# Kernel tuning notes

Hardware: AMD Instinct MI355X
Metric: run time of the kernel (lower is better)

Reference implementation:

```python
import jax, jax.numpy as jnp
import numpy as np

EPS = 1e-8
SQRT_EPS_LOSS = 1e-6


def setup_inputs() -> dict:
    key = jax.random.key(0)
    ks = jax.random.split(key, 8)
    n_vars, n_clauses, n_edges, n_graphs = 500_000, 2_000_000, 6_000_000, 256
    dim, k = 128, 8
    x = jax.random.normal(ks[0], (n_vars, dim), jnp.float32)
    polarity = jnp.where(jax.random.bernoulli(ks[1], 0.5, (n_edges,)), 1.0, -1.0).astype(jnp.float32)
    variable_indices = jax.random.randint(ks[2], (n_edges,), 0, n_vars)
    clause_indices = jax.random.randint(ks[3], (n_edges,), 0, n_clauses)
    clause_batch = jnp.sort(jax.random.randint(ks[4], (n_clauses,), 0, n_graphs))
    W1 = jax.random.normal(ks[5], (dim, dim), jnp.float32) / np.sqrt(dim).astype(np.float32)
    b1 = jnp.zeros((dim,), jnp.float32)
    W2 = jax.random.normal(ks[6], (dim, k), jnp.float32) / np.sqrt(dim).astype(np.float32)
    b2 = jnp.zeros((k,), jnp.float32)
    return dict(x=x, polarity=polarity, variable_indices=variable_indices,
                clause_indices=clause_indices, clause_batch=clause_batch,
                W1=W1, b1=b1, W2=W2, b2=b2, n_graphs=n_graphs)


def reference(x, polarity, variable_indices, clause_indices, clause_batch, W1, b1, W2, b2, n_graphs):
    n_clauses = clause_batch.shape[0]
    k = W2.shape[1]

    # variables_output MLP: Linear -> ReLU -> Linear, [n_vars, k]
    logits = jax.nn.relu(x @ W1 + b1) @ W2 + b2

    # softplus_mixed_loss: gather literals along edges, scatter-sum into clauses
    lit = logits[variable_indices] * polarity[:, None]                      # [E, k]
    clause_sum = jax.ops.segment_sum(jax.nn.softplus(lit), clause_indices,
                                     num_segments=n_clauses)                # [C, k]
    clause_val = jnp.exp(-clause_sum)
    per_clause_loss = clause_val * (-jnp.log(1.0 - clause_val + EPS))       # [C, k]

    # per-graph soft loss
    per_graph_loss = jax.ops.segment_sum(per_clause_loss, clause_batch,
                                         num_segments=n_graphs)             # [G, k]
    per_graph_loss = jnp.sqrt(per_graph_loss + SQRT_EPS_LOSS) - np.float32(np.sqrt(SQRT_EPS_LOSS))

    costs = jnp.square(jnp.arange(1, k + 1, dtype=jnp.float32))             # [k]
    sorted_desc = -jnp.sort(-per_graph_loss, axis=-1)                       # descending sort per graph
    logit_loss = jnp.sum(sorted_desc * costs) / jnp.sum(costs)              # scalar

    # hard assignment check
    logits_hard = jnp.where(logits > 0, 1.0, -1.0)
    edge_hard = logits_hard[variable_indices] * polarity[:, None]           # [E, k]
    clauses_hard = jax.ops.segment_max(edge_hard, clause_indices,
                                       num_segments=n_clauses)              # amax per clause
    graphs_hard = jax.ops.segment_min(clauses_hard, clause_batch,
                                      num_segments=n_graphs)                # amin per graph
    solved = jnp.any(graphs_hard > 0.5, axis=1)                             # [G] bool

    return logit_loss, solved
```

## Files before the change

kernel.cpp:

```cpp
#include <hip/hip_runtime.h>
#include <hip/hip_bf16.h>

#define DIM 128
#define K 8
#define EPS 1e-8f
#define SQRT_EPS 1e-6f

#define CB 512
#define CSHIFT 9
#define NBMAX 4096
#define MAXSLOT 32
#define SARR_CAP 2560

#define TV1 8192
#define NT1MAX 1024
#define NKV 512
#define VSH 10
#define TB 4096
#define MAXTV 4
#define NKC 64
#define TC 4096
#define MAXTC 32

typedef __attribute__((ext_vector_type(8))) short bf16x8;
typedef __attribute__((ext_vector_type(4))) float f32x4;

__device__ inline short bfc(float f) {
    union { __hip_bfloat16 h; short s; } u;
    u.h = __float2bfloat16(f);
    return u.s;
}

#define LDW 136
#define NW 8

__global__ __launch_bounds__(512) void prep_kernel(
    const float* __restrict__ W1, const float* __restrict__ W2,
    unsigned short* __restrict__ w1tg, unsigned short* __restrict__ w2tg)
{
    const int t = threadIdx.x;
    for (int i = t; i < DIM * DIM; i += 512) {
        int r = i >> 7, c = i & 127;
        w1tg[c * DIM + r] = (unsigned short)bfc(W1[i]);
    }
    for (int i = t; i < 16 * DIM; i += 512) {
        int c = i >> 7, j = i & 127;
        w2tg[c * DIM + j] = (c < 8) ? (unsigned short)bfc(W2[j * 8 + c])
                                    : (unsigned short)0;
    }
}

__global__ __launch_bounds__(512) void mlp_kernel(
    const float* __restrict__ x, const unsigned short* __restrict__ w1tg,
    const float* __restrict__ b1, const unsigned short* __restrict__ w2tg,
    const float* __restrict__ b2, uint2* __restrict__ lfp8, int n_vars)
{
    __shared__ __align__(16) short w1t[DIM][LDW];
    __shared__ __align__(16) short w2t[16][LDW];
    __shared__ __align__(16) short hlds[NW][16][LDW];
    __shared__ __align__(16) float lout[NW][16][8];

    const int t = threadIdx.x;
    const int wave = t >> 6, lane = t & 63;
    const int lr = lane & 15, lg = lane >> 4;

    for (int i = t; i < DIM * DIM / 8; i += 512) {
        int row = i >> 4, col8 = (i & 15) * 8;
        *(bf16x8*)&w1t[row][col8] = *(const bf16x8*)&w1tg[row * DIM + col8];
    }
    for (int i = t; i < 16 * DIM / 8; i += 512) {
        int row = i >> 4, col8 = (i & 15) * 8;
        *(bf16x8*)&w2t[row][col8] = *(const bf16x8*)&w2tg[row * DIM + col8];
    }
    __syncthreads();

    const int rbase = blockIdx.x * 256 + wave * 32;

    bf16x8 a[2][4];
    #pragma unroll
    for (int rt = 0; rt < 2; ++rt) {
        int row = rbase + rt * 16 + lr;
        bool ok = row < n_vars;
        const float* xp = x + (size_t)row * DIM + lg * 8;
        #pragma unroll
        for (int kt = 0; kt < 4; ++kt) {
            bf16x8 av = {0,0,0,0,0,0,0,0};
            if (ok) {
                float4 f0 = *(const float4*)(xp + kt * 32);
                float4 f1 = *(const float4*)(xp + kt * 32 + 4);
                av[0]=bfc(f0.x); av[1]=bfc(f0.y); av[2]=bfc(f0.z); av[3]=bfc(f0.w);
                av[4]=bfc(f1.x); av[5]=bfc(f1.y); av[6]=bfc(f1.z); av[7]=bfc(f1.w);
            }
            a[rt][kt] = av;
        }
    }

    bf16x8 bb[4];
    #pragma unroll
    for (int kt = 0; kt < 4; ++kt)
        bb[kt] = *(const bf16x8*)&w2t[lr][kt * 32 + lg * 8];
    float b2v = (lr < 8) ? b2[lr] : 0.f;

    #pragma unroll
    for (int rt = 0; rt < 2; ++rt) {
        #pragma unroll
        for (int n = 0; n < 8; ++n) {
            f32x4 acc = {0.f, 0.f, 0.f, 0.f};
            #pragma unroll
            for (int kt = 0; kt < 4; ++kt) {
                bf16x8 bf = *(const bf16x8*)&w1t[n * 16 + lr][kt * 32 + lg * 8];
                acc = __builtin_amdgcn_mfma_f32_16x16x32_bf16(a[rt][kt], bf, acc, 0, 0, 0);
            }
            float bcol = b1[n * 16 + lr];
            #pragma unroll
            for (int r = 0; r < 4; ++r) {
                float h = fmaxf(acc[r] + bcol, 0.f);
                hlds[wave][lg * 4 + r][n * 16 + lr] = bfc(h);
            }
        }
        f32x4 acc2 = {0.f, 0.f, 0.f, 0.f};
        #pragma unroll
        for (int kt = 0; kt < 4; ++kt) {
            bf16x8 af = *(const bf16x8*)&hlds[wave][lr][kt * 32 + lg * 8];
            acc2 = __builtin_amdgcn_mfma_f32_16x16x32_bf16(af, bb[kt], acc2, 0, 0, 0);
        }
        if (lr < 8) {
            #pragma unroll
            for (int r = 0; r < 4; ++r)
                lout[wave][lg * 4 + r][lr] = acc2[r] + b2v;
        }
        if (lane < 16) {
            int row = rbase + rt * 16 + lane;
            if (row < n_vars) {
                const float* f = lout[wave][lane];
                unsigned lo = 0u, hi = 0u;
                lo = __builtin_amdgcn_cvt_pk_fp8_f32(f[0], f[1], lo, false);
                lo = __builtin_amdgcn_cvt_pk_fp8_f32(f[2], f[3], lo, true);
                hi = __builtin_amdgcn_cvt_pk_fp8_f32(f[4], f[5], hi, false);
                hi = __builtin_amdgcn_cvt_pk_fp8_f32(f[6], f[7], hi, true);
                lfp8[row] = make_uint2(lo, hi);
            }
        }
    }
}


__global__ __launch_bounds__(256) void histV_kernel(
    const int* __restrict__ vi, unsigned* __restrict__ histV, int n_edges)
{
    __shared__ unsigned hl[NKV];
    const int t = threadIdx.x, b = blockIdx.x;
    for (int i = t; i < NKV; i += 256) hl[i] = 0u;
    __syncthreads();
    const int e0 = b * TV1, e1 = min(e0 + TV1, n_edges);
    for (int e = e0 + t; e < e1; e += 256)
        atomicAdd(&hl[((unsigned)vi[e]) >> VSH], 1u);
    __syncthreads();
    for (int i = t; i < NKV; i += 256) histV[(size_t)i * NT1MAX + b] = hl[i];
}

__global__ __launch_bounds__(256) void scanrowV_kernel(
    unsigned* __restrict__ hist, unsigned* __restrict__ btotal)
{
    const int t = threadIdx.x;
    const size_t base = (size_t)blockIdx.x * NT1MAX + t * 4;
    uint4 v = *(const uint4*)(hist + base);
    unsigned pre0 = 0, pre1 = v.x, pre2 = v.x + v.y, pre3 = v.x + v.y + v.z;
    unsigned run = pre3 + v.w;
    __shared__ unsigned ts[256];
    ts[t] = run;
    __syncthreads();
    for (int off = 1; off < 256; off <<= 1) {
        unsigned xv = (t >= off) ? ts[t - off] : 0u;
        __syncthreads();
        ts[t] += xv;
        __syncthreads();
    }
    unsigned ex = ts[t] - run;
    uint4 o = {ex + pre0, ex + pre1, ex + pre2, ex + pre3};
    *(uint4*)(hist + base) = o;
    if (t == 255) btotal[blockIdx.x] = ts[255];
}

__global__ void baseV_kernel(const unsigned* __restrict__ tv,
                             unsigned* __restrict__ bv)
{
    if (threadIdx.x == 0) {
        unsigned r = 0;
        for (int k = 0; k < NKV; ++k) { bv[k] = r; r += tv[k]; }
        bv[NKV] = r;
    }
}

__global__ __launch_bounds__(256) void scatterV_kernel(
    const int* __restrict__ ci, const int* __restrict__ vi,
    const float* __restrict__ pol, const unsigned* __restrict__ histV,
    const unsigned* __restrict__ baseV, unsigned* __restrict__ A, int n_edges)
{
    __shared__ unsigned sa[TV1];
    __shared__ unsigned short bmap[TV1];
    __shared__ unsigned h[NKV], lst[NKV], h2[NKV], gst[NKV];
    __shared__ unsigned ts[256];
    const int t = threadIdx.x, b = blockIdx.x;
    for (int i = t; i < NKV; i += 256) h[i] = 0u;
    __syncthreads();
    const int e0 = b * TV1, e1 = min(e0 + TV1, n_edges), n = e1 - e0;
    for (int e = e0 + t; e < e1; e += 256)
        atomicAdd(&h[((unsigned)vi[e]) >> VSH], 1u);
    __syncthreads();
    unsigned a0 = h[2 * t], a1 = h[2 * t + 1];
    unsigned run = a0 + a1;
    ts[t] = run;
    __syncthreads();
    for (int off = 1; off < 256; off <<= 1) {
        unsigned xv = (t >= off) ? ts[t - off] : 0u;
        __syncthreads();
        ts[t] += xv;
        __syncthreads();
    }
    unsigned ex = ts[t] - run;
    lst[2 * t] = ex; lst[2 * t + 1] = ex + a0;
    h2[2 * t] = ex;  h2[2 * t + 1] = ex + a0;
    __syncthreads();
    for (int e = e0 + t; e < e1; e += 256) {
        unsigned c = (unsigned)ci[e];
        unsigned v = (unsigned)vi[e];
        unsigned neg = (pol[e] < 0.f) ? 1u : 0u;
        unsigned k = v >> VSH;
        unsigned p = atomicAdd(&h2[k], 1u);
        sa[p] = c | (neg << 21) | ((v & ((1u << VSH) - 1u)) << 22);
        bmap[p] = (unsigned short)k;
    }
    for (int i = t; i < NKV; i += 256)
        gst[i] = baseV[i] + histV[(size_t)i * NT1MAX + b];
    __syncthreads();
    for (int s = t; s < n; s += 256) {
        unsigned k = bmap[s];
        A[gst[k] + (s - lst[k])] = sa[s];
    }
}


__global__ __launch_bounds__(256) void histB_kernel(
    const unsigned* __restrict__ A, const unsigned* __restrict__ baseV,
    unsigned* __restrict__ histB)
{
    __shared__ unsigned h[NKC];
    const int t = threadIdx.x;
    const int vg = blockIdx.x / MAXTV, i = blockIdx.x % MAXTV;
    const unsigned slo = baseV[vg], shi = baseV[vg + 1];
    const unsigned t0 = slo + (unsigned)i * TB;
    if (t0 >= shi) return;
    const unsigned t1 = min(t0 + TB, shi);
    if (t < NKC) h[t] = 0u;
    __syncthreads();
    for (unsigned e = t0 + t; e < t1; e += 256)
        atomicAdd(&h[(A[e] & 0x1FFFFFu) >> 15], 1u);
    __syncthreads();
    if (t < NKC) histB[(size_t)t * (NKV * MAXTV) + blockIdx.x] = h[t];
}

__global__ __launch_bounds__(256) void scanrowB_kernel(
    unsigned* __restrict__ hist, unsigned* __restrict__ btotal)
{
    const int t = threadIdx.x;
    const size_t base = (size_t)blockIdx.x * (NKV * MAXTV) + t * 8;
    uint4 v0 = *(const uint4*)(hist + base);
    uint4 v1 = *(const uint4*)(hist + base + 4);
    unsigned p0 = 0, p1 = v0.x, p2 = p1 + v0.y, p3 = p2 + v0.z, p4 = p3 + v0.w;
    unsigned p5 = p4 + v1.x, p6 = p5 + v1.y, p7 = p6 + v1.z;
    unsigned run = p7 + v1.w;
    __shared__ unsigned ts[256];
    ts[t] = run;
    __syncthreads();
    for (int off = 1; off < 256; off <<= 1) {
        unsigned xv = (t >= off) ? ts[t - off] : 0u;
        __syncthreads();
        ts[t] += xv;
        __syncthreads();
    }
    unsigned ex = ts[t] - run;
    uint4 o0 = {ex + p0, ex + p1, ex + p2, ex + p3};
    uint4 o1 = {ex + p4, ex + p5, ex + p6, ex + p7};
    *(uint4*)(hist + base) = o0;
    *(uint4*)(hist + base + 4) = o1;
    if (t == 255) btotal[blockIdx.x] = ts[255];
}

__global__ void baseB_kernel(const unsigned* __restrict__ tb,
                             unsigned* __restrict__ bb)
{
    if (threadIdx.x == 0) {
        unsigned r = 0;
        for (int k = 0; k < NKC; ++k) { bb[k] = r; r += tb[k]; }
        bb[NKC] = r;
    }
}

__global__ __launch_bounds__(256) void scatterB_kernel(
    const unsigned* __restrict__ A, const uint2* __restrict__ lfp8,
    const unsigned* __restrict__ baseV, const unsigned* __restrict__ histB,
    const unsigned* __restrict__ baseB, unsigned short* __restrict__ B1,
    uint2* __restrict__ B2, int n_vars)
{
    __shared__ uint2 slice[1 << VSH];
    __shared__ unsigned short st1[TB];
    __shared__ uint2 st2[TB];
    __shared__ unsigned char bmap[TB];
    __shared__ unsigned h[NKC], lst[NKC], h2[NKC], gst[NKC];
    const int t = threadIdx.x;
    const int vg = blockIdx.x / MAXTV, i = blockIdx.x % MAXTV;
    const unsigned slo = baseV[vg], shi = baseV[vg + 1];
    const unsigned t0 = slo + (unsigned)i * TB;
    if (t0 >= shi) return;
    const unsigned t1 = min(t0 + TB, shi);
    const int n = (int)(t1 - t0);
    for (int s = t; s < (1 << VSH); s += 256) {
        int v = (vg << VSH) + s;
        slice[s] = (v < n_vars) ? lfp8[v] : make_uint2(0u, 0u);
    }
    if (t < NKC) h[t] = 0u;
    __syncthreads();
    for (unsigned e = t0 + t; e < t1; e += 256)
        atomicAdd(&h[(A[e] & 0x1FFFFFu) >> 15], 1u);
    __syncthreads();
    if (t == 0) {
        unsigned r = 0;
        for (int k = 0; k < NKC; ++k) { lst[k] = r; h2[k] = r; r += h[k]; }
    }
    __syncthreads();
    for (unsigned e = t0 + t; e < t1; e += 256) {
        unsigned a = A[e];
        unsigned c = a & 0x1FFFFFu;
        unsigned k = c >> 15;
        unsigned p = atomicAdd(&h2[k], 1u);
        uint2 g = slice[a >> 22];
        unsigned sm = ((a >> 21) & 1u) * 0x80808080u;
        g.x ^= sm; g.y ^= sm;
        st1[p] = (unsigned short)(c & 0x7FFFu);
        st2[p] = g;
        bmap[p] = (unsigned char)k;
    }
    if (t < NKC) gst[t] = baseB[t] + histB[(size_t)t * (NKV * MAXTV) + blockIdx.x];
    __syncthreads();
    for (int s = t; s < n; s += 256) {
        unsigned k = bmap[s];
        unsigned pos = gst[k] + (s - lst[k]);
        B1[pos] = st1[s];
        B2[pos] = st2[s];
    }
}


__global__ __launch_bounds__(256) void histC_kernel(
    const unsigned short* __restrict__ B1, const unsigned* __restrict__ baseB,
    unsigned* __restrict__ histC)
{
    __shared__ unsigned h[64];
    const int t = threadIdx.x;
    const int k1 = blockIdx.x / MAXTC, i = blockIdx.x % MAXTC;
    const unsigned slo = baseB[k1], shi = baseB[k1 + 1];
    const unsigned t0 = slo + (unsigned)i * TC;
    if (t0 >= shi) return;
    const unsigned t1 = min(t0 + TC, shi);
    if (t < 64) h[t] = 0u;
    __syncthreads();
    for (unsigned e = t0 + t; e < t1; e += 256)
        atomicAdd(&h[((unsigned)B1[e] >> 9) & 63u], 1u);
    __syncthreads();
    if (t < 64) histC[(size_t)(k1 * 64 + t) * MAXTC + i] = h[t];
}

__global__ __launch_bounds__(256) void scanrowC_kernel(
    unsigned* __restrict__ histC, unsigned* __restrict__ ctotal)
{
    const int rid = blockIdx.x * 256 + threadIdx.x;
    unsigned r = 0;
    for (int i = 0; i < MAXTC; ++i) {
        unsigned v = histC[(size_t)rid * MAXTC + i];
        histC[(size_t)rid * MAXTC + i] = r;
        r += v;
    }
    ctotal[rid] = r;
}

__global__ __launch_bounds__(256) void bbase_kernel(
    const unsigned* __restrict__ ctotal, unsigned* __restrict__ bbase, int nb)
{
    const int t = threadIdx.x;
    unsigned loc[16];
    unsigned run = 0;
    #pragma unroll
    for (int it = 0; it < 16; ++it) {
        int idx = t * 16 + it;
        unsigned v = (idx < 4096) ? ctotal[idx] : 0u;
        loc[it] = run;
        run += v;
    }
    __shared__ unsigned ts[256];
    ts[t] = run;
    __syncthreads();
    for (int off = 1; off < 256; off <<= 1) {
        unsigned xv = (t >= off) ? ts[t - off] : 0u;
        __syncthreads();
        ts[t] += xv;
        __syncthreads();
    }
    unsigned ex = ts[t] - run;
    #pragma unroll
    for (int it = 0; it < 16; ++it) {
        int idx = t * 16 + it;
        if (idx <= nb) bbase[idx] = ex + loc[it];
    }
}

__global__ __launch_bounds__(256) void scatterC_kernel(
    const unsigned short* __restrict__ B1, const uint2* __restrict__ B2,
    const unsigned* __restrict__ baseB, const unsigned* __restrict__ histC,
    const unsigned* __restrict__ bbase, unsigned short* __restrict__ sortedS,
    uint2* __restrict__ sortedL)
{
    __shared__ unsigned short st1[TC];
    __shared__ uint2 st2[TC];
    __shared__ unsigned char bmap[TC];
    __shared__ unsigned h[64], lst[64], h2[64], gst[64];
    const int t = threadIdx.x;
    const int k1 = blockIdx.x / MAXTC, i = blockIdx.x % MAXTC;
    const unsigned slo = baseB[k1], shi = baseB[k1 + 1];
    const unsigned t0 = slo + (unsigned)i * TC;
    if (t0 >= shi) return;
    const unsigned t1 = min(t0 + TC, shi);
    const int n = (int)(t1 - t0);
    if (t < 64) h[t] = 0u;
    __syncthreads();
    for (unsigned e = t0 + t; e < t1; e += 256)
        atomicAdd(&h[((unsigned)B1[e] >> 9) & 63u], 1u);
    __syncthreads();
    if (t == 0) {
        unsigned r = 0;
        for (int k = 0; k < 64; ++k) { lst[k] = r; h2[k] = r; r += h[k]; }
    }
    __syncthreads();
    for (unsigned e = t0 + t; e < t1; e += 256) {
        unsigned b = (unsigned)B1[e];
        unsigned k2 = (b >> 9) & 63u;
        unsigned p = atomicAdd(&h2[k2], 1u);
        st1[p] = (unsigned short)(b & 0x1FFu);
        st2[p] = B2[e];
        bmap[p] = (unsigned char)k2;
    }
    if (t < 64) {
        unsigned cbk = (unsigned)(k1 * 64 + t);
        gst[t] = bbase[cbk] + histC[(size_t)cbk * MAXTC + i];
    }
    __syncthreads();
    for (int s = t; s < n; s += 256) {
        unsigned k = bmap[s];
        unsigned pos = gst[k] + (s - lst[k]);
        sortedS[pos] = st1[s];
        sortedL[pos] = st2[s];
    }
}

__global__ __launch_bounds__(256) void bucket_kernel(
    const unsigned short* __restrict__ sortedS, const uint2* __restrict__ sortedL,
    const unsigned* __restrict__ bbase, const int* __restrict__ clause_batch,
    float* __restrict__ per_graph, unsigned* __restrict__ gmask,
    int n_clauses, int n_graphs)
{
    __shared__ uint2 sarrL[SARR_CAP];
    __shared__ unsigned cnt[CB];
    __shared__ unsigned cst[CB + 1];
    __shared__ float sp[256];
    __shared__ float pg[MAXSLOT * K];
    __shared__ unsigned pmask[MAXSLOT];
    __shared__ unsigned wtot[4];
    __shared__ int sh_ghi;

    const int t = threadIdx.x;
    const int lane = t & 63, wv = t >> 6;
    const int bkt = blockIdx.x;
    const int c_base = bkt << CSHIFT;
    const int n_cl = min(CB, n_clauses - c_base);
    const int g_lo = clause_batch[c_base];

    {
        float v = __builtin_amdgcn_cvt_f32_fp8((unsigned)t, 0);
        sp[t] = fmaxf(v, 0.f) + __logf(1.f + __expf(-fabsf(v)));
    }
    for (int i = t; i < CB; i += 256) cnt[i] = 0u;
    for (int i = t; i < MAXSLOT * K; i += 256) pg[i] = 0.f;
    if (t < MAXSLOT) pmask[t] = 0xFFu;
    if (t == 0) sh_ghi = clause_batch[c_base + n_cl - 1];
    __syncthreads();

    const unsigned lo = bbase[bkt], hi = bbase[bkt + 1];
    const int ne = (int)(hi - lo);

    float loss0[K], loss1[K];
    unsigned msk0 = 0u, msk1 = 0u;
    bool have0 = false, have1 = false;

    if (ne <= SARR_CAP) {
        for (unsigned e = lo + t; e < hi; e += 256)
            atomicAdd(&cnt[sortedS[e] & 511u], 1u);
        __syncthreads();
        unsigned a0 = cnt[2 * t], a1 = cnt[2 * t + 1];
        unsigned run = a0 + a1;
        unsigned incl = run;
        #pragma unroll
        for (int off = 1; off < 64; off <<= 1) {
            unsigned v = __shfl_up(incl, off, 64);
            if (lane >= off) incl += v;
        }
        if (lane == 63) wtot[wv] = incl;
        __syncthreads();
        unsigned wpre = 0;
        #pragma unroll
        for (int w = 0; w < 3; ++w) if (w < wv) wpre += wtot[w];
        unsigned ex = wpre + incl - run;
        cst[2 * t] = ex; cst[2 * t + 1] = ex + a0;
        cnt[2 * t] = ex; cnt[2 * t + 1] = ex + a0;
        if (t == 255) cst[CB] = ex + run;
        __syncthreads();
        for (unsigned e = lo + t; e < hi; e += 256) {
            unsigned cl = sortedS[e] & 511u;
            unsigned p = atomicAdd(&cnt[cl], 1u);
            sarrL[p] = sortedL[e];
        }
        __syncthreads();
        #pragma unroll
        for (int oc = 0; oc < 2; ++oc) {
            int cl = 2 * t + oc;
            if (cl >= n_cl) continue;
            unsigned s0 = cst[cl];
            int n = (int)(cst[cl + 1] - s0);
            float sums[K] = {0.f, 0.f, 0.f, 0.f, 0.f, 0.f, 0.f, 0.f};
            unsigned ormask = 0u;
            for (int base = 0; base < n; base += 8) {
                int m = min(8, n - base);
                uint2 gs[8];
                for (int i2 = 0; i2 < m; ++i2) gs[i2] = sarrL[s0 + base + i2];
                for (int i2 = 0; i2 < m; ++i2) {
                    #pragma unroll
                    for (int j = 0; j < 4; ++j) {
                        unsigned b0 = (gs[i2].x >> (8 * j)) & 0xFFu;
                        unsigned b1 = (gs[i2].y >> (8 * j)) & 0xFFu;
                        sums[j]     += sp[b0];
                        sums[j + 4] += sp[b1];
                        ormask |= (b0 - 1u < 0x7Fu) ? (1u << j) : 0u;
                        ormask |= (b1 - 1u < 0x7Fu) ? (1u << (j + 4)) : 0u;
                    }
                }
            }
            float* lss = oc ? loss1 : loss0;
            #pragma unroll
            for (int j = 0; j < K; ++j) {
                float cv = __expf(-sums[j]);
                lss[j] = cv * (-__logf(1.f - cv + EPS));
            }
            if (oc) { msk1 = ormask; have1 = true; }
            else    { msk0 = ormask; have0 = true; }
        }
    } else {
        float* acc = (float*)sarrL;
        unsigned* fmsk = cnt;
        for (int i = t; i < CB * K; i += 256) acc[i] = 0.f;
        for (int i = t; i < CB; i += 256) fmsk[i] = 0u;
        __syncthreads();
        for (unsigned e = lo + t; e < hi; e += 256) {
            unsigned cl = sortedS[e] & 511u;
            uint2 g = sortedL[e];
            unsigned gt0 = 0u;
            #pragma unroll
            for (int j = 0; j < 4; ++j) {
                unsigned b0 = (g.x >> (8 * j)) & 0xFFu;
                unsigned b1 = (g.y >> (8 * j)) & 0xFFu;
                atomicAdd(&acc[cl * K + j], sp[b0]);
                atomicAdd(&acc[cl * K + j + 4], sp[b1]);
                gt0 |= (b0 - 1u < 0x7Fu) ? (1u << j) : 0u;
                gt0 |= (b1 - 1u < 0x7Fu) ? (1u << (j + 4)) : 0u;
            }
            atomicOr(&fmsk[cl], gt0);
        }
        __syncthreads();
        #pragma unroll
        for (int oc = 0; oc < 2; ++oc) {
            int cl = 2 * t + oc;
            if (cl >= n_cl) continue;
            float* lss = oc ? loss1 : loss0;
            #pragma unroll
            for (int j = 0; j < K; ++j) {
                float cv = __expf(-acc[cl * K + j]);
                lss[j] = cv * (-__logf(1.f - cv + EPS));
            }
            if (oc) { msk1 = fmsk[cl]; have1 = true; }
            else    { msk0 = fmsk[cl]; have0 = true; }
        }
    }

    if (have0) {
        int slot0 = clause_batch[c_base + 2 * t] - g_lo;
        int slot1 = have1 ? (clause_batch[c_base + 2 * t + 1] - g_lo) : -1;
        if (have1 && slot1 == slot0) {
            #pragma unroll
            for (int j = 0; j < K; ++j) loss0[j] += loss1[j];
            msk0 &= msk1;
            have1 = false;
        }
        if (slot0 < MAXSLOT) {
            #pragma unroll
            for (int j = 0; j < K; ++j) atomicAdd(&pg[slot0 * K + j], loss0[j]);
            atomicAnd(&pmask[slot0], msk0);
        } else {
            #pragma unroll
            for (int j = 0; j < K; ++j) atomicAdd(&per_graph[(size_t)(g_lo + slot0) * K + j], loss0[j]);
            atomicAnd(&gmask[g_lo + slot0], msk0);
        }
        if (have1) {
            if (slot1 < MAXSLOT) {
                #pragma unroll
                for (int j = 0; j < K; ++j) atomicAdd(&pg[slot1 * K + j], loss1[j]);
                atomicAnd(&pmask[slot1], msk1);
            } else {
                #pragma unroll
                for (int j = 0; j < K; ++j) atomicAdd(&per_graph[(size_t)(g_lo + slot1) * K + j], loss1[j]);
                atomicAnd(&gmask[g_lo + slot1], msk1);
            }
        }
    }
    __syncthreads();

    const int nslots = min(sh_ghi - g_lo + 1, MAXSLOT);
    if (t < nslots * K) {
        int s = t >> 3, j = t & 7;
        atomicAdd(&per_graph[(size_t)(g_lo + s) * K + j], pg[s * K + j]);
    }
    if (t < nslots) atomicAnd(&gmask[g_lo + t], pmask[t]);
}

__global__ __launch_bounds__(256) void final_kernel(
    const float* __restrict__ per_graph, const unsigned* __restrict__ gmask,
    int n_graphs, float* __restrict__ out)
{
    const int t = threadIdx.x;
    float dot = 0.f;
    if (t < n_graphs) {
        float v[K];
        #pragma unroll
        for (int j = 0; j < K; ++j)
            v[j] = sqrtf(per_graph[(size_t)t * K + j] + SQRT_EPS) - sqrtf(SQRT_EPS);
        #pragma unroll
        for (int i = 1; i < K; ++i) {
            float key = v[i];
            int j = i - 1;
            while (j >= 0 && v[j] < key) { v[j + 1] = v[j]; --j; }
            v[j + 1] = key;
        }
        #pragma unroll
        for (int i = 0; i < K; ++i)
            dot = fmaf(v[i], (float)((i + 1) * (i + 1)), dot);
        out[1 + t] = (gmask[t] & 0xFFu) ? 1.f : 0.f;
    }
    __shared__ float red[256];
    red[t] = dot;
    __syncthreads();
    for (int s = 128; s >= 1; s >>= 1) {
        if (t < s) red[t] += red[t + s];
        __syncthreads();
    }
    if (t == 0) out[0] = red[0] * (1.f / 204.f);
}

extern "C" void kernel_launch(void* const* d_in, const int* in_sizes, int n_in,
                              void* d_out, int out_size, void* d_ws, size_t ws_size,
                              hipStream_t stream) {
    const float* x   = (const float*)d_in[0];
    const float* pol = (const float*)d_in[1];
    const int* vi    = (const int*)d_in[2];
    const int* ci    = (const int*)d_in[3];
    const int* cb    = (const int*)d_in[4];
    const float* W1  = (const float*)d_in[5];
    const float* b1  = (const float*)d_in[6];
    const float* W2  = (const float*)d_in[7];
    const float* b2  = (const float*)d_in[8];

    const int n_vars    = in_sizes[0] / DIM;
    const int n_edges   = in_sizes[1];
    const int n_clauses = in_sizes[4];
    const int n_graphs  = out_size - 1;
    const int nb        = (n_clauses + CB - 1) / CB;
    const int nt1       = (n_edges + TV1 - 1) / TV1;

    char* ws = (char*)d_ws;
    size_t off = 0;
    auto alloc = [&](size_t bytes) { char* p = ws + off; off += (bytes + 255) & ~(size_t)255; return p; };
    uint2*    lfp8   = (uint2*)alloc((size_t)n_vars * 8);
    unsigned* A      = (unsigned*)alloc((size_t)n_edges * 4);
    unsigned short* B1 = (unsigned short*)alloc((size_t)n_edges * 2);
    uint2*    B2     = (uint2*)alloc((size_t)n_edges * 8);
    uint2*    sortedL= (uint2*)alloc((size_t)n_edges * 8);
    unsigned* histV  = (unsigned*)alloc((size_t)NKV * NT1MAX * 4);
    unsigned* histB  = (unsigned*)alloc((size_t)NKC * NKV * MAXTV * 4);
    unsigned* histC  = (unsigned*)alloc((size_t)4096 * MAXTC * 4);
    unsigned* btotalV= (unsigned*)alloc((size_t)(NKV + 1) * 4);
    unsigned* baseV  = (unsigned*)alloc((size_t)(NKV + 1) * 4);
    unsigned* btotalB= (unsigned*)alloc((size_t)(NKC + 1) * 4);
    unsigned* baseB  = (unsigned*)alloc((size_t)(NKC + 1) * 4);
    unsigned* ctotal = (unsigned*)alloc((size_t)4096 * 4);
    unsigned* bbase  = (unsigned*)alloc((size_t)(NBMAX + 1) * 4);
    float*    per_graph = (float*)alloc((size_t)n_graphs * K * 4);
    unsigned* gmask  = (unsigned*)alloc((size_t)n_graphs * 4);
    unsigned short* w1tg = (unsigned short*)alloc((size_t)DIM * DIM * 2);
    unsigned short* w2tg = (unsigned short*)alloc((size_t)16 * DIM * 2);
    unsigned short* sortedS = (unsigned short*)A;

    hipMemsetAsync(histV, 0, (size_t)NKV * NT1MAX * 4, stream);
    hipMemsetAsync(histB, 0, (size_t)NKC * NKV * MAXTV * 4, stream);
    hipMemsetAsync(histC, 0, (size_t)4096 * MAXTC * 4, stream);
    hipMemsetAsync(per_graph, 0, (size_t)n_graphs * K * 4, stream);
    hipMemsetAsync(gmask, 0xFF, (size_t)n_graphs * 4, stream);

    prep_kernel<<<1, 512, 0, stream>>>(W1, W2, w1tg, w2tg);
    mlp_kernel<<<(n_vars + 255) / 256, 512, 0, stream>>>(x, w1tg, b1, w2tg, b2,
                                                         lfp8, n_vars);

    histV_kernel<<<nt1, 256, 0, stream>>>(vi, histV, n_edges);
    scanrowV_kernel<<<NKV, 256, 0, stream>>>(histV, btotalV);
    baseV_kernel<<<1, 64, 0, stream>>>(btotalV, baseV);
    scatterV_kernel<<<nt1, 256, 0, stream>>>(ci, vi, pol, histV, baseV, A, n_edges);

    histB_kernel<<<NKV * MAXTV, 256, 0, stream>>>(A, baseV, histB);
    scanrowB_kernel<<<NKC, 256, 0, stream>>>(histB, btotalB);
    baseB_kernel<<<1, 64, 0, stream>>>(btotalB, baseB);
    scatterB_kernel<<<NKV * MAXTV, 256, 0, stream>>>(A, lfp8, baseV, histB, baseB,
                                                     B1, B2, n_vars);

    histC_kernel<<<NKC * MAXTC, 256, 0, stream>>>(B1, baseB, histC);
    scanrowC_kernel<<<16, 256, 0, stream>>>(histC, ctotal);
    bbase_kernel<<<1, 256, 0, stream>>>(ctotal, bbase, nb);
    scatterC_kernel<<<NKC * MAXTC, 256, 0, stream>>>(B1, B2, baseB, histC, bbase,
                                                     sortedS, sortedL);

    bucket_kernel<<<nb, 256, 0, stream>>>(sortedS, sortedL, bbase, cb,
                                          per_graph, gmask, n_clauses, n_graphs);
    final_kernel<<<1, 256, 0, stream>>>(per_graph, gmask, n_graphs, (float*)d_out);
}
```

Before: 456.5 us.

## Halve clause bucket and sort tile sizes to increase block-level parallelism

Shrinks the clause bucket from 512 to 256 clauses, so each thread in the bucket kernel handles one clause instead of two. It also halves the edge tiles in the three radix-sort passes, doubling block counts and widening the per-pass histograms and scans to match. The MLP kernel now reads W2 straight from global memory instead of staging it in shared memory. The aim is more blocks and less shared memory per block for better occupancy, at the cost of more partial histograms to scan and more per-graph atomics from smaller buckets.

```diff
diff --git a/kernel.cpp b/kernel.cpp
--- a/kernel.cpp
+++ b/kernel.cpp
@@ -6,21 +6,22 @@
 #define EPS 1e-8f
 #define SQRT_EPS 1e-6f
 
-#define CB 512
-#define CSHIFT 9
-#define NBMAX 4096
+#define CB 256
+#define CSHIFT 8
+#define NBMAX 8192
 #define MAXSLOT 32
-#define SARR_CAP 2560
-
-#define TV1 8192
-#define NT1MAX 1024
+#define SARR_CAP 1280
+
+#define TV1 4096
+#define NT1MAX 2048
 #define NKV 512
 #define VSH 10
-#define TB 4096
-#define MAXTV 4
+#define TB 2048
+#define MAXTV 8
 #define NKC 64
-#define TC 4096
-#define MAXTC 32
+#define TC 2048
+#define MAXTC 64
+#define NFB 128
 
 typedef __attribute__((ext_vector_type(8))) short bf16x8;
 typedef __attribute__((ext_vector_type(4))) float f32x4;
@@ -56,7 +57,6 @@
     const float* __restrict__ b2, uint2* __restrict__ lfp8, int n_vars)
 {
     __shared__ __align__(16) short w1t[DIM][LDW];
-    __shared__ __align__(16) short w2t[16][LDW];
     __shared__ __align__(16) short hlds[NW][16][LDW];
     __shared__ __align__(16) float lout[NW][16][8];
 
@@ -67,10 +67,6 @@
     for (int i = t; i < DIM * DIM / 8; i += 512) {
         int row = i >> 4, col8 = (i & 15) * 8;
         *(bf16x8*)&w1t[row][col8] = *(const bf16x8*)&w1tg[row * DIM + col8];
-    }
-    for (int i = t; i < 16 * DIM / 8; i += 512) {
-        int row = i >> 4, col8 = (i & 15) * 8;
-        *(bf16x8*)&w2t[row][col8] = *(const bf16x8*)&w2tg[row * DIM + col8];
     }
     __syncthreads();
 
@@ -98,7 +94,7 @@
     bf16x8 bb[4];
     #pragma unroll
     for (int kt = 0; kt < 4; ++kt)
-        bb[kt] = *(const bf16x8*)&w2t[lr][kt * 32 + lg * 8];
+        bb[kt] = *(const bf16x8*)&w2tg[lr * DIM + kt * 32 + lg * 8];
     float b2v = (lr < 8) ? b2[lr] : 0.f;
 
     #pragma unroll
@@ -163,10 +159,12 @@
     unsigned* __restrict__ hist, unsigned* __restrict__ btotal)
 {
     const int t = threadIdx.x;
-    const size_t base = (size_t)blockIdx.x * NT1MAX + t * 4;
-    uint4 v = *(const uint4*)(hist + base);
-    unsigned pre0 = 0, pre1 = v.x, pre2 = v.x + v.y, pre3 = v.x + v.y + v.z;
-    unsigned run = pre3 + v.w;
+    const size_t base = (size_t)blockIdx.x * NT1MAX + t * 8;
+    uint4 v0 = *(const uint4*)(hist + base);
+    uint4 v1 = *(const uint4*)(hist + base + 4);
+    unsigned p0 = 0, p1 = v0.x, p2 = p1 + v0.y, p3 = p2 + v0.z, p4 = p3 + v0.w;
+    unsigned p5 = p4 + v1.x, p6 = p5 + v1.y, p7 = p6 + v1.z;
+    unsigned run = p7 + v1.w;
     __shared__ unsigned ts[256];
     ts[t] = run;
     __syncthreads();
@@ -177,8 +175,10 @@
         __syncthreads();
     }
     unsigned ex = ts[t] - run;
-    uint4 o = {ex + pre0, ex + pre1, ex + pre2, ex + pre3};
-    *(uint4*)(hist + base) = o;
+    uint4 o0 = {ex + p0, ex + p1, ex + p2, ex + p3};
+    uint4 o1 = {ex + p4, ex + p5, ex + p6, ex + p7};
+    *(uint4*)(hist + base) = o0;
+    *(uint4*)(hist + base + 4) = o1;
     if (t == 255) btotal[blockIdx.x] = ts[255];
 }
 
@@ -264,12 +264,17 @@
     unsigned* __restrict__ hist, unsigned* __restrict__ btotal)
 {
     const int t = threadIdx.x;
-    const size_t base = (size_t)blockIdx.x * (NKV * MAXTV) + t * 8;
-    uint4 v0 = *(const uint4*)(hist + base);
-    uint4 v1 = *(const uint4*)(hist + base + 4);
-    unsigned p0 = 0, p1 = v0.x, p2 = p1 + v0.y, p3 = p2 + v0.z, p4 = p3 + v0.w;
-    unsigned p5 = p4 + v1.x, p6 = p5 + v1.y, p7 = p6 + v1.z;
-    unsigned run = p7 + v1.w;
+    const size_t base = (size_t)blockIdx.x * (NKV * MAXTV) + t * 16;
+    unsigned v[16];
+    #pragma unroll
+    for (int q = 0; q < 4; ++q) {
+        uint4 vv = *(const uint4*)(hist + base + q * 4);
+        v[q*4+0]=vv.x; v[q*4+1]=vv.y; v[q*4+2]=vv.z; v[q*4+3]=vv.w;
+    }
+    unsigned pre[16];
+    unsigned run = 0;
+    #pragma unroll
+    for (int q = 0; q < 16; ++q) { pre[q] = run; run += v[q]; }
     __shared__ unsigned ts[256];
     ts[t] = run;
     __syncthreads();
@@ -280,10 +285,11 @@
         __syncthreads();
     }
     unsigned ex = ts[t] - run;
-    uint4 o0 = {ex + p0, ex + p1, ex + p2, ex + p3};
-    uint4 o1 = {ex + p4, ex + p5, ex + p6, ex + p7};
-    *(uint4*)(hist + base) = o0;
-    *(uint4*)(hist + base + 4) = o1;
+    #pragma unroll
+    for (int q = 0; q < 4; ++q) {
+        uint4 o = {ex + pre[q*4+0], ex + pre[q*4+1], ex + pre[q*4+2], ex + pre[q*4+3]};
+        *(uint4*)(hist + base + q * 4) = o;
+    }
     if (t == 255) btotal[blockIdx.x] = ts[255];
 }
 
@@ -356,19 +362,19 @@
     const unsigned short* __restrict__ B1, const unsigned* __restrict__ baseB,
     unsigned* __restrict__ histC)
 {
-    __shared__ unsigned h[64];
+    __shared__ unsigned h[NFB];
     const int t = threadIdx.x;
     const int k1 = blockIdx.x / MAXTC, i = blockIdx.x % MAXTC;
     const unsigned slo = baseB[k1], shi = baseB[k1 + 1];
     const unsigned t0 = slo + (unsigned)i * TC;
     if (t0 >= shi) return;
     const unsigned t1 = min(t0 + TC, shi);
-    if (t < 64) h[t] = 0u;
+    if (t < NFB) h[t] = 0u;
     __syncthreads();
     for (unsigned e = t0 + t; e < t1; e += 256)
-        atomicAdd(&h[((unsigned)B1[e] >> 9) & 63u], 1u);
-    __syncthreads();
-    if (t < 64) histC[(size_t)(k1 * 64 + t) * MAXTC + i] = h[t];
+        atomicAdd(&h[((unsigned)B1[e] >> CSHIFT) & (NFB - 1u)], 1u);
+    __syncthreads();
+    if (t < NFB) histC[(size_t)(k1 * NFB + t) * MAXTC + i] = h[t];
 }
 
 __global__ __launch_bounds__(256) void scanrowC_kernel(
@@ -388,12 +394,12 @@
     const unsigned* __restrict__ ctotal, unsigned* __restrict__ bbase, int nb)
 {
     const int t = threadIdx.x;
-    unsigned loc[16];
+    unsigned loc[32];
     unsigned run = 0;
     #pragma unroll
-    for (int it = 0; it < 16; ++it) {
-        int idx = t * 16 + it;
-        unsigned v = (idx < 4096) ? ctotal[idx] : 0u;
+    for (int it = 0; it < 32; ++it) {
+        int idx = t * 32 + it;
+        unsigned v = (idx < 8192) ? ctotal[idx] : 0u;
         loc[it] = run;
         run += v;
     }
@@ -408,8 +414,8 @@
     }
     unsigned ex = ts[t] - run;
     #pragma unroll
-    for (int it = 0; it < 16; ++it) {
-        int idx = t * 16 + it;
+    for (int it = 0; it < 32; ++it) {
+        int idx = t * 32 + it;
         if (idx <= nb) bbase[idx] = ex + loc[it];
     }
 }
@@ -423,7 +429,7 @@
     __shared__ unsigned short st1[TC];
     __shared__ uint2 st2[TC];
     __shared__ unsigned char bmap[TC];
-    __shared__ unsigned h[64], lst[64], h2[64], gst[64];
+    __shared__ unsigned h[NFB], lst[NFB], h2[NFB], gst[NFB];
     const int t = threadIdx.x;
     const int k1 = blockIdx.x / MAXTC, i = blockIdx.x % MAXTC;
     const unsigned slo = baseB[k1], shi = baseB[k1 + 1];
@@ -431,26 +437,26 @@
     if (t0 >= shi) return;
     const unsigned t1 = min(t0 + TC, shi);
     const int n = (int)(t1 - t0);
-    if (t < 64) h[t] = 0u;
+    if (t < NFB) h[t] = 0u;
     __syncthreads();
     for (unsigned e = t0 + t; e < t1; e += 256)
-        atomicAdd(&h[((unsigned)B1[e] >> 9) & 63u], 1u);
+        atomicAdd(&h[((unsigned)B1[e] >> CSHIFT) & (NFB - 1u)], 1u);
     __syncthreads();
     if (t == 0) {
         unsigned r = 0;
-        for (int k = 0; k < 64; ++k) { lst[k] = r; h2[k] = r; r += h[k]; }
+        for (int k = 0; k < NFB; ++k) { lst[k] = r; h2[k] = r; r += h[k]; }
     }
     __syncthreads();
     for (unsigned e = t0 + t; e < t1; e += 256) {
         unsigned b = (unsigned)B1[e];
-        unsigned k2 = (b >> 9) & 63u;
+        unsigned k2 = (b >> CSHIFT) & (NFB - 1u);
         unsigned p = atomicAdd(&h2[k2], 1u);
-        st1[p] = (unsigned short)(b & 0x1FFu);
+        st1[p] = (unsigned short)(b & (CB - 1u));
         st2[p] = B2[e];
         bmap[p] = (unsigned char)k2;
     }
-    if (t < 64) {
-        unsigned cbk = (unsigned)(k1 * 64 + t);
+    if (t < NFB) {
+        unsigned cbk = (unsigned)(k1 * NFB + t);
         gst[t] = bbase[cbk] + histC[(size_t)cbk * MAXTC + i];
     }
     __syncthreads();
@@ -488,26 +494,25 @@
         float v = __builtin_amdgcn_cvt_f32_fp8((unsigned)t, 0);
         sp[t] = fmaxf(v, 0.f) + __logf(1.f + __expf(-fabsf(v)));
     }
-    for (int i = t; i < CB; i += 256) cnt[i] = 0u;
+    cnt[t] = 0u;
+    if (t < MAXSLOT) { pmask[t] = 0xFFu; }
     for (int i = t; i < MAXSLOT * K; i += 256) pg[i] = 0.f;
-    if (t < MAXSLOT) pmask[t] = 0xFFu;
     if (t == 0) sh_ghi = clause_batch[c_base + n_cl - 1];
     __syncthreads();
 
     const unsigned lo = bbase[bkt], hi = bbase[bkt + 1];
     const int ne = (int)(hi - lo);
 
-    float loss0[K], loss1[K];
-    unsigned msk0 = 0u, msk1 = 0u;
-    bool have0 = false, have1 = false;
+    float loss0[K];
+    unsigned msk0 = 0u;
+    bool have0 = false;
 
     if (ne <= SARR_CAP) {
         for (unsigned e = lo + t; e < hi; e += 256)
-            atomicAdd(&cnt[sortedS[e] & 511u], 1u);
-        __syncthreads();
-        unsigned a0 = cnt[2 * t], a1 = cnt[2 * t + 1];
-        unsigned run = a0 + a1;
-        unsigned incl = run;
+            atomicAdd(&cnt[sortedS[e] & (CB - 1u)], 1u);
+        __syncthreads();
+        unsigned a0 = cnt[t];
+        unsigned incl = a0;
         #pragma unroll
         for (int off = 1; off < 64; off <<= 1) {
             unsigned v = __shfl_up(incl, off, 64);
@@ -518,23 +523,20 @@
         unsigned wpre = 0;
         #pragma unroll
         for (int w = 0; w < 3; ++w) if (w < wv) wpre += wtot[w];
-        unsigned ex = wpre + incl - run;
-        cst[2 * t] = ex; cst[2 * t + 1] = ex + a0;
-        cnt[2 * t] = ex; cnt[2 * t + 1] = ex + a0;
-        if (t == 255) cst[CB] = ex + run;
+        unsigned ex = wpre + incl - a0;
+        cst[t] = ex;
+        cnt[t] = ex;
+        if (t == 255) cst[CB] = ex + a0;
         __syncthreads();
         for (unsigned e = lo + t; e < hi; e += 256) {
-            unsigned cl = sortedS[e] & 511u;
+            unsigned cl = sortedS[e] & (CB - 1u);
             unsigned p = atomicAdd(&cnt[cl], 1u);
             sarrL[p] = sortedL[e];
         }
         __syncthreads();
-        #pragma unroll
-        for (int oc = 0; oc < 2; ++oc) {
-            int cl = 2 * t + oc;
-            if (cl >= n_cl) continue;
-            unsigned s0 = cst[cl];
-            int n = (int)(cst[cl + 1] - s0);
+        if (t < n_cl) {
+            unsigned s0 = cst[t];
+            int n = (int)(cst[t + 1] - s0);
             float sums[K] = {0.f, 0.f, 0.f, 0.f, 0.f, 0.f, 0.f, 0.f};
             unsigned ormask = 0u;
             for (int base = 0; base < n; base += 8) {
@@ -553,23 +555,22 @@
                     }
                 }
             }
-            float* lss = oc ? loss1 : loss0;
             #pragma unroll
             for (int j = 0; j < K; ++j) {
                 float cv = __expf(-sums[j]);
-                lss[j] = cv * (-__logf(1.f - cv + EPS));
+                loss0[j] = cv * (-__logf(1.f - cv + EPS));
             }
-            if (oc) { msk1 = ormask; have1 = true; }
-            else    { msk0 = ormask; have0 = true; }
+            msk0 = ormask;
+            have0 = true;
         }
     } else {
         float* acc = (float*)sarrL;
-        unsigned* fmsk = cnt;
+        __shared__ unsigned fmsk[CB];
         for (int i = t; i < CB * K; i += 256) acc[i] = 0.f;
-        for (int i = t; i < CB; i += 256) fmsk[i] = 0u;
+        fmsk[t] = 0u;
         __syncthreads();
         for (unsigned e = lo + t; e < hi; e += 256) {
-            unsigned cl = sortedS[e] & 511u;
+            unsigned cl = sortedS[e] & (CB - 1u);
             uint2 g = sortedL[e];
             unsigned gt0 = 0u;
             #pragma unroll
@@ -584,30 +585,19 @@
             atomicOr(&fmsk[cl], gt0);
         }
         __syncthreads();
-        #pragma unroll
-        for (int oc = 0; oc < 2; ++oc) {
-            int cl = 2 * t + oc;
-            if (cl >= n_cl) continue;
-            float* lss = oc ? loss1 : loss0;
+        if (t < n_cl) {
             #pragma unroll
             for (int j = 0; j < K; ++j) {
-                float cv = __expf(-acc[cl * K + j]);
-                lss[j] = cv * (-__logf(1.f - cv + EPS));
+                float cv = __expf(-acc[t * K + j]);
+                loss0[j] = cv * (-__logf(1.f - cv + EPS));
             }
-            if (oc) { msk1 = fmsk[cl]; have1 = true; }
-            else    { msk0 = fmsk[cl]; have0 = true; }
+            msk0 = fmsk[t];
+            have0 = true;
         }
     }
 
     if (have0) {
-        int slot0 = clause_batch[c_base + 2 * t] - g_lo;
-        int slot1 = have1 ? (clause_batch[c_base + 2 * t + 1] - g_lo) : -1;
-        if (have1 && slot1 == slot0) {
-            #pragma unroll
-            for (int j = 0; j < K; ++j) loss0[j] += loss1[j];
-            msk0 &= msk1;
-            have1 = false;
-        }
+        int slot0 = clause_batch[c_base + t] - g_lo;
         if (slot0 < MAXSLOT) {
             #pragma unroll
             for (int j = 0; j < K; ++j) atomicAdd(&pg[slot0 * K + j], loss0[j]);
@@ -616,17 +606,6 @@
             #pragma unroll
             for (int j = 0; j < K; ++j) atomicAdd(&per_graph[(size_t)(g_lo + slot0) * K + j], loss0[j]);
             atomicAnd(&gmask[g_lo + slot0], msk0);
-        }
-        if (have1) {
-            if (slot1 < MAXSLOT) {
-                #pragma unroll
-                for (int j = 0; j < K; ++j) atomicAdd(&pg[slot1 * K + j], loss1[j]);
-                atomicAnd(&pmask[slot1], msk1);
-            } else {
-                #pragma unroll
-                for (int j = 0; j < K; ++j) atomicAdd(&per_graph[(size_t)(g_lo + slot1) * K + j], loss1[j]);
-                atomicAnd(&gmask[g_lo + slot1], msk1);
-            }
         }
     }
     __syncthreads();
@@ -702,12 +681,12 @@
     uint2*    sortedL= (uint2*)alloc((size_t)n_edges * 8);
     unsigned* histV  = (unsigned*)alloc((size_t)NKV * NT1MAX * 4);
     unsigned* histB  = (unsigned*)alloc((size_t)NKC * NKV * MAXTV * 4);
-    unsigned* histC  = (unsigned*)alloc((size_t)4096 * MAXTC * 4);
+    unsigned* histC  = (unsigned*)alloc((size_t)8192 * MAXTC * 4);
     unsigned* btotalV= (unsigned*)alloc((size_t)(NKV + 1) * 4);
     unsigned* baseV  = (unsigned*)alloc((size_t)(NKV + 1) * 4);
     unsigned* btotalB= (unsigned*)alloc((size_t)(NKC + 1) * 4);
     unsigned* baseB  = (unsigned*)alloc((size_t)(NKC + 1) * 4);
-    unsigned* ctotal = (unsigned*)alloc((size_t)4096 * 4);
+    unsigned* ctotal = (unsigned*)alloc((size_t)8192 * 4);
     unsigned* bbase  = (unsigned*)alloc((size_t)(NBMAX + 1) * 4);
     float*    per_graph = (float*)alloc((size_t)n_graphs * K * 4);
     unsigned* gmask  = (unsigned*)alloc((size_t)n_graphs * 4);
@@ -717,7 +696,7 @@
 
     hipMemsetAsync(histV, 0, (size_t)NKV * NT1MAX * 4, stream);
     hipMemsetAsync(histB, 0, (size_t)NKC * NKV * MAXTV * 4, stream);
-    hipMemsetAsync(histC, 0, (size_t)4096 * MAXTC * 4, stream);
+    hipMemsetAsync(histC, 0, (size_t)8192 * MAXTC * 4, stream);
     hipMemsetAsync(per_graph, 0, (size_t)n_graphs * K * 4, stream);
     hipMemsetAsync(gmask, 0xFF, (size_t)n_graphs * 4, stream);
 
@@ -737,7 +716,7 @@
                                                      B1, B2, n_vars);
 
     histC_kernel<<<NKC * MAXTC, 256, 0, stream>>>(B1, baseB, histC);
-    scanrowC_kernel<<<16, 256, 0, stream>>>(histC, ctotal);
+    scanrowC_kernel<<<32, 256, 0, stream>>>(histC, ctotal);
     bbase_kernel<<<1, 256, 0, stream>>>(ctotal, bbase, nb);
     scatterC_kernel<<<NKC * MAXTC, 256, 0, stream>>>(B1, B2, baseB, histC, bbase,
                                                      sortedS, sortedL);
```

Result: slower. 487.4 us (+6.8%).

## Fuse MLP with vertex histogram and compute bucket bases inside scatter kernels

Applied to the files above, without the earlier changes.

The vertex-bucket histogram now runs as extra blocks of the MLP launch, so the MLP and histogram work share one grid and can overlap. scatterV and scatterB each rebuild the bucket base offsets locally from the totals instead of reading a separately computed array. The serial base kernels still run, so the overall launch count stays about the same. The bucket kernel also keeps its edges in registers (up to 10 per thread) so the second pass does not reload them from global memory, at the cost of more register pressure. It also drops the shared copy of W2 and reads it straight from global memory.

```diff
diff --git a/kernel.cpp b/kernel.cpp
--- a/kernel.cpp
+++ b/kernel.cpp
@@ -11,6 +11,7 @@
 #define NBMAX 4096
 #define MAXSLOT 32
 #define SARR_CAP 2560
+#define MAXE 10
 
 #define TV1 8192
 #define NT1MAX 1024
@@ -50,27 +51,38 @@
     }
 }
 
-__global__ __launch_bounds__(512) void mlp_kernel(
+__global__ __launch_bounds__(512) void mlp_histV_kernel(
     const float* __restrict__ x, const unsigned short* __restrict__ w1tg,
     const float* __restrict__ b1, const unsigned short* __restrict__ w2tg,
-    const float* __restrict__ b2, uint2* __restrict__ lfp8, int n_vars)
+    const float* __restrict__ b2, uint2* __restrict__ lfp8, int n_vars,
+    const int* __restrict__ vi, unsigned* __restrict__ histV, int n_edges,
+    int mlpB)
 {
     __shared__ __align__(16) short w1t[DIM][LDW];
-    __shared__ __align__(16) short w2t[16][LDW];
     __shared__ __align__(16) short hlds[NW][16][LDW];
     __shared__ __align__(16) float lout[NW][16][8];
-
-    const int t = threadIdx.x;
+    __shared__ unsigned hl[NKV];
+
+    const int t = threadIdx.x;
+
+    if ((int)blockIdx.x >= mlpB) {
+        const int b = (int)blockIdx.x - mlpB;
+        for (int i = t; i < NKV; i += 512) hl[i] = 0u;
+        __syncthreads();
+        const int e0 = b * TV1, e1 = min(e0 + TV1, n_edges);
+        for (int e = e0 + t; e < e1; e += 512)
+            atomicAdd(&hl[((unsigned)vi[e]) >> VSH], 1u);
+        __syncthreads();
+        for (int i = t; i < NKV; i += 512) histV[(size_t)i * NT1MAX + b] = hl[i];
+        return;
+    }
+
     const int wave = t >> 6, lane = t & 63;
     const int lr = lane & 15, lg = lane >> 4;
 
     for (int i = t; i < DIM * DIM / 8; i += 512) {
         int row = i >> 4, col8 = (i & 15) * 8;
         *(bf16x8*)&w1t[row][col8] = *(const bf16x8*)&w1tg[row * DIM + col8];
-    }
-    for (int i = t; i < 16 * DIM / 8; i += 512) {
-        int row = i >> 4, col8 = (i & 15) * 8;
-        *(bf16x8*)&w2t[row][col8] = *(const bf16x8*)&w2tg[row * DIM + col8];
     }
     __syncthreads();
 
@@ -98,7 +110,7 @@
     bf16x8 bb[4];
     #pragma unroll
     for (int kt = 0; kt < 4; ++kt)
-        bb[kt] = *(const bf16x8*)&w2t[lr][kt * 32 + lg * 8];
+        bb[kt] = *(const bf16x8*)&w2tg[lr * DIM + kt * 32 + lg * 8];
     float b2v = (lr < 8) ? b2[lr] : 0.f;
 
     #pragma unroll
@@ -144,21 +156,6 @@
     }
 }
 
-
-__global__ __launch_bounds__(256) void histV_kernel(
-    const int* __restrict__ vi, unsigned* __restrict__ histV, int n_edges)
-{
-    __shared__ unsigned hl[NKV];
-    const int t = threadIdx.x, b = blockIdx.x;
-    for (int i = t; i < NKV; i += 256) hl[i] = 0u;
-    __syncthreads();
-    const int e0 = b * TV1, e1 = min(e0 + TV1, n_edges);
-    for (int e = e0 + t; e < e1; e += 256)
-        atomicAdd(&hl[((unsigned)vi[e]) >> VSH], 1u);
-    __syncthreads();
-    for (int i = t; i < NKV; i += 256) histV[(size_t)i * NT1MAX + b] = hl[i];
-}
-
 __global__ __launch_bounds__(256) void scanrowV_kernel(
     unsigned* __restrict__ hist, unsigned* __restrict__ btotal)
 {
@@ -182,26 +179,32 @@
     if (t == 255) btotal[blockIdx.x] = ts[255];
 }
 
-__global__ void baseV_kernel(const unsigned* __restrict__ tv,
-                             unsigned* __restrict__ bv)
-{
-    if (threadIdx.x == 0) {
-        unsigned r = 0;
-        for (int k = 0; k < NKV; ++k) { bv[k] = r; r += tv[k]; }
-        bv[NKV] = r;
-    }
-}
-
 __global__ __launch_bounds__(256) void scatterV_kernel(
     const int* __restrict__ ci, const int* __restrict__ vi,
     const float* __restrict__ pol, const unsigned* __restrict__ histV,
-    const unsigned* __restrict__ baseV, unsigned* __restrict__ A, int n_edges)
+    const unsigned* __restrict__ btotalV, unsigned* __restrict__ A, int n_edges)
 {
     __shared__ unsigned sa[TV1];
     __shared__ unsigned short bmap[TV1];
     __shared__ unsigned h[NKV], lst[NKV], h2[NKV], gst[NKV];
+    __shared__ unsigned baseVl[NKV];
     __shared__ unsigned ts[256];
     const int t = threadIdx.x, b = blockIdx.x;
+
+    {
+        unsigned v0 = btotalV[2 * t], v1 = btotalV[2 * t + 1];
+        unsigned run = v0 + v1;
+        ts[t] = run;
+        __syncthreads();
+        for (int off = 1; off < 256; off <<= 1) {
+            unsigned xv = (t >= off) ? ts[t - off] : 0u;
+            __syncthreads();
+            ts[t] += xv;
+            __syncthreads();
+        }
+        unsigned ex = ts[t] - run;
+        baseVl[2 * t] = ex; baseVl[2 * t + 1] = ex + v0;
+    }
     for (int i = t; i < NKV; i += 256) h[i] = 0u;
     __syncthreads();
     const int e0 = b * TV1, e1 = min(e0 + TV1, n_edges), n = e1 - e0;
@@ -232,7 +235,7 @@
         bmap[p] = (unsigned short)k;
     }
     for (int i = t; i < NKV; i += 256)
-        gst[i] = baseV[i] + histV[(size_t)i * NT1MAX + b];
+        gst[i] = baseVl[i] + histV[(size_t)i * NT1MAX + b];
     __syncthreads();
     for (int s = t; s < n; s += 256) {
         unsigned k = bmap[s];
@@ -258,6 +261,16 @@
         atomicAdd(&h[(A[e] & 0x1FFFFFu) >> 15], 1u);
     __syncthreads();
     if (t < NKC) histB[(size_t)t * (NKV * MAXTV) + blockIdx.x] = h[t];
+}
+
+__global__ void baseV_pub_kernel(const unsigned* __restrict__ tv,
+                                 unsigned* __restrict__ bv)
+{
+    if (threadIdx.x == 0) {
+        unsigned r = 0;
+        for (int k = 0; k < NKV; ++k) { bv[k] = r; r += tv[k]; }
+        bv[NKV] = r;
+    }
 }
 
 __global__ __launch_bounds__(256) void scanrowB_kernel(
@@ -287,27 +300,17 @@
     if (t == 255) btotal[blockIdx.x] = ts[255];
 }
 
-__global__ void baseB_kernel(const unsigned* __restrict__ tb,
-                             unsigned* __restrict__ bb)
-{
-    if (threadIdx.x == 0) {
-        unsigned r = 0;
-        for (int k = 0; k < NKC; ++k) { bb[k] = r; r += tb[k]; }
-        bb[NKC] = r;
-    }
-}
-
 __global__ __launch_bounds__(256) void scatterB_kernel(
     const unsigned* __restrict__ A, const uint2* __restrict__ lfp8,
     const unsigned* __restrict__ baseV, const unsigned* __restrict__ histB,
-    const unsigned* __restrict__ baseB, unsigned short* __restrict__ B1,
+    const unsigned* __restrict__ btotalB, unsigned short* __restrict__ B1,
     uint2* __restrict__ B2, int n_vars)
 {
     __shared__ uint2 slice[1 << VSH];
     __shared__ unsigned short st1[TB];
     __shared__ uint2 st2[TB];
     __shared__ unsigned char bmap[TB];
-    __shared__ unsigned h[NKC], lst[NKC], h2[NKC], gst[NKC];
+    __shared__ unsigned h[NKC], lst[NKC], h2[NKC], gst[NKC], baseBl[NKC];
     const int t = threadIdx.x;
     const int vg = blockIdx.x / MAXTV, i = blockIdx.x % MAXTV;
     const unsigned slo = baseV[vg], shi = baseV[vg + 1];
@@ -315,6 +318,13 @@
     if (t0 >= shi) return;
     const unsigned t1 = min(t0 + TB, shi);
     const int n = (int)(t1 - t0);
+    if (t < NKC) h[t] = btotalB[t];
+    __syncthreads();
+    if (t == 0) {
+        unsigned r = 0;
+        for (int k = 0; k < NKC; ++k) { baseBl[k] = r; r += h[k]; }
+    }
+    __syncthreads();
     for (int s = t; s < (1 << VSH); s += 256) {
         int v = (vg << VSH) + s;
         slice[s] = (v < n_vars) ? lfp8[v] : make_uint2(0u, 0u);
@@ -341,13 +351,23 @@
         st2[p] = g;
         bmap[p] = (unsigned char)k;
     }
-    if (t < NKC) gst[t] = baseB[t] + histB[(size_t)t * (NKV * MAXTV) + blockIdx.x];
+    if (t < NKC) gst[t] = baseBl[t] + histB[(size_t)t * (NKV * MAXTV) + blockIdx.x];
     __syncthreads();
     for (int s = t; s < n; s += 256) {
         unsigned k = bmap[s];
         unsigned pos = gst[k] + (s - lst[k]);
         B1[pos] = st1[s];
         B2[pos] = st2[s];
+    }
+}
+
+__global__ void baseB_pub_kernel(const unsigned* __restrict__ tb,
+                                 unsigned* __restrict__ bb)
+{
+    if (threadIdx.x == 0) {
+        unsigned r = 0;
+        for (int k = 0; k < NKC; ++k) { bb[k] = r; r += tb[k]; }
+        bb[NKC] = r;
     }
 }
 
@@ -502,8 +522,16 @@
     bool have0 = false, have1 = false;
 
     if (ne <= SARR_CAP) {
-        for (unsigned e = lo + t; e < hi; e += 256)
-            atomicAdd(&cnt[sortedS[e] & 511u], 1u);
+        unsigned short myS[MAXE];
+        uint2 myL[MAXE];
+        #pragma unroll
+        for (int u = 0; u < MAXE; ++u) {
+            unsigned e = lo + t + 256u * u;
+            bool ok = e < hi;
+            myS[u] = ok ? sortedS[e] : (unsigned short)0xFFFFu;
+            myL[u] = ok ? sortedL[e] : make_uint2(0u, 0u);
+            if (ok) atomicAdd(&cnt[myS[u] & 511u], 1u);
+        }
         __syncthreads();
         unsigned a0 = cnt[2 * t], a1 = cnt[2 * t + 1];
         unsigned run = a0 + a1;
@@ -523,10 +551,12 @@
         cnt[2 * t] = ex; cnt[2 * t + 1] = ex + a0;
         if (t == 255) cst[CB] = ex + run;
         __syncthreads();
-        for (unsigned e = lo + t; e < hi; e += 256) {
-            unsigned cl = sortedS[e] & 511u;
-            unsigned p = atomicAdd(&cnt[cl], 1u);
-            sarrL[p] = sortedL[e];
+        #pragma unroll
+        for (int u = 0; u < MAXE; ++u) {
+            if (myS[u] != (unsigned short)0xFFFFu) {
+                unsigned p = atomicAdd(&cnt[myS[u] & 511u], 1u);
+                sarrL[p] = myL[u];
+            }
         }
         __syncthreads();
         #pragma unroll
@@ -691,6 +721,7 @@
     const int n_graphs  = out_size - 1;
     const int nb        = (n_clauses + CB - 1) / CB;
     const int nt1       = (n_edges + TV1 - 1) / TV1;
+    const int mlpB      = (n_vars + 255) / 256;
 
     char* ws = (char*)d_ws;
     size_t off = 0;
@@ -722,18 +753,18 @@
     hipMemsetAsync(gmask, 0xFF, (size_t)n_graphs * 4, stream);
 
     prep_kernel<<<1, 512, 0, stream>>>(W1, W2, w1tg, w2tg);
-    mlp_kernel<<<(n_vars + 255) / 256, 512, 0, stream>>>(x, w1tg, b1, w2tg, b2,
-                                                         lfp8, n_vars);
-
-    histV_kernel<<<nt1, 256, 0, stream>>>(vi, histV, n_edges);
+    mlp_histV_kernel<<<mlpB + nt1, 512, 0, stream>>>(x, w1tg, b1, w2tg, b2,
+                                                     lfp8, n_vars, vi, histV,
+                                                     n_edges, mlpB);
+
     scanrowV_kernel<<<NKV, 256, 0, stream>>>(histV, btotalV);
-    baseV_kernel<<<1, 64, 0, stream>>>(btotalV, baseV);
-    scatterV_kernel<<<nt1, 256, 0, stream>>>(ci, vi, pol, histV, baseV, A, n_edges);
+    baseV_pub_kernel<<<1, 64, 0, stream>>>(btotalV, baseV);
+    scatterV_kernel<<<nt1, 256, 0, stream>>>(ci, vi, pol, histV, btotalV, A, n_edges);
 
     histB_kernel<<<NKV * MAXTV, 256, 0, stream>>>(A, baseV, histB);
     scanrowB_kernel<<<NKC, 256, 0, stream>>>(histB, btotalB);
-    baseB_kernel<<<1, 64, 0, stream>>>(btotalB, baseB);
-    scatterB_kernel<<<NKV * MAXTV, 256, 0, stream>>>(A, lfp8, baseV, histB, baseB,
+    baseB_pub_kernel<<<1, 64, 0, stream>>>(btotalB, baseB);
+    scatterB_kernel<<<NKV * MAXTV, 256, 0, stream>>>(A, lfp8, baseV, histB, btotalB,
                                                      B1, B2, n_vars);
 
     histC_kernel<<<NKC * MAXTC, 256, 0, stream>>>(B1, baseB, histC);
```

After: 453.0 us. About the same (-0.8%).
